# Optimization experiments

Hardware: AMD Instinct MI355X
Metric: run time of the kernel (lower is better)

## Reference

```python
import jax, jax.numpy as jnp
import numpy as np

# FP8 E4M3 constants (per FP8Handler)
E4M3_MAX = 240.0          # max_normal
MANTISSA_SCALE = 8.0      # 2 ** mantissa_bits (3)
SCALE_EPS = 1e-10


def setup_inputs() -> dict:
    key = jax.random.key(0)
    k1, k2, k3 = jax.random.split(key, 3)
    B, S, D_IN, D_OUT = 4, 2048, 4096, 4096
    x = jax.random.normal(k1, (B, S, D_IN), dtype=jnp.float32)
    weight = jax.random.normal(k2, (D_OUT, D_IN), dtype=jnp.float32)
    bias = jax.random.normal(k3, (D_OUT,), dtype=jnp.float32)
    return {"x": x, "weight": weight, "bias": bias}


def _fp8_e4m3_quant_dequant(w, scale):
    # FP8Handler.quantize_tensor + _simulate_e4m3_precision
    s = jnp.clip(w / scale, -E4M3_MAX, E4M3_MAX)
    s = s.astype(jnp.float16).astype(jnp.float32)  # fp16 round-trip
    q = jnp.round(s * MANTISSA_SCALE) / MANTISSA_SCALE  # mantissa truncation
    q = jnp.clip(q, -E4M3_MAX, E4M3_MAX)
    return q * scale


def reference(x, weight, bias):
    # FP8Quantizer.compute_scale: per-tensor max-abs, margin=0, fresh history
    amax = jnp.max(jnp.abs(weight))
    scale = jnp.maximum(amax / E4M3_MAX, SCALE_EPS)
    qw = _fp8_e4m3_quant_dequant(weight, scale)  # [out, in]
    # F.linear(x, qw, bias): x [b, s, in] @ qw.T [in, out] + bias
    return jnp.einsum('bsi,oi->bso', x, qw) + bias
```

## Files before the change

kernel.cpp:

```cpp
#include <hip/hip_runtime.h>
#include <hip/hip_bf16.h>
#include <hip/hip_fp16.h>

#define E4M3_MAX 240.0f

typedef __attribute__((ext_vector_type(8))) __bf16 bf16x8;
typedef __attribute__((ext_vector_type(16))) float f32x16;
typedef unsigned short ushort_t;

__device__ __forceinline__ void gload_lds16(const void* g, void* l) {
  __builtin_amdgcn_global_load_lds(
      (const __attribute__((address_space(1))) void*)g,
      (__attribute__((address_space(3))) void*)l,
      16, 0, 0);
}

__global__ void amax_abs_kernel(const float* __restrict__ w, int n4,
                                unsigned* __restrict__ amax_bits) {
  float m = 0.0f;
  const float4* w4 = (const float4*)w;
  int stride = gridDim.x * blockDim.x;
  for (int i = blockIdx.x * blockDim.x + threadIdx.x; i < n4; i += stride) {
    float4 v = w4[i];
    m = fmaxf(m, fmaxf(fmaxf(fabsf(v.x), fabsf(v.y)),
                       fmaxf(fabsf(v.z), fabsf(v.w))));
  }
  for (int off = 32; off > 0; off >>= 1)
    m = fmaxf(m, __shfl_down(m, off, 64));
  __shared__ float smax[4];
  int l = threadIdx.x & 63, wv = threadIdx.x >> 6;
  if (l == 0) smax[wv] = m;
  __syncthreads();
  if (threadIdx.x == 0) {
    float bm = fmaxf(fmaxf(smax[0], smax[1]), fmaxf(smax[2], smax[3]));
    atomicMax(amax_bits, __float_as_uint(bm));
  }
}

__global__ void quant_weight_kernel(const float* __restrict__ w,
                                    const unsigned* __restrict__ amax_bits,
                                    ushort_t* __restrict__ qw, int n4) {
  float amax = __uint_as_float(*amax_bits);
  float scale = fmaxf(amax / E4M3_MAX, 1e-10f);
  const float4* w4 = (const float4*)w;
  ushort4* q4 = (ushort4*)qw;
  int stride = gridDim.x * blockDim.x;
  for (int i = blockIdx.x * blockDim.x + threadIdx.x; i < n4; i += stride) {
    float4 v = w4[i];
    float r[4] = {v.x, v.y, v.z, v.w};
    ushort_t o[4];
#pragma unroll
    for (int j = 0; j < 4; ++j) {
      float s = fminf(fmaxf(r[j] / scale, -E4M3_MAX), E4M3_MAX);
      s = __half2float(__float2half(s));
      float q = rintf(s * 8.0f) * 0.125f;
      q = fminf(fmaxf(q, -E4M3_MAX), E4M3_MAX);
      __hip_bfloat16 h = __float2bfloat16(q * scale);
      o[j] = *(ushort_t*)&h;
    }
    ushort4 ov = {o[0], o[1], o[2], o[3]};
    q4[i] = ov;
  }
}

__global__ void cvt_bf16_kernel(const float* __restrict__ x,
                                ushort_t* __restrict__ xb, int n4) {
  const float4* x4 = (const float4*)x;
  ushort4* o4 = (ushort4*)xb;
  int stride = gridDim.x * blockDim.x;
  for (int i = blockIdx.x * blockDim.x + threadIdx.x; i < n4; i += stride) {
    float4 v = x4[i];
    __hip_bfloat16 h0 = __float2bfloat16(v.x);
    __hip_bfloat16 h1 = __float2bfloat16(v.y);
    __hip_bfloat16 h2 = __float2bfloat16(v.z);
    __hip_bfloat16 h3 = __float2bfloat16(v.w);
    ushort4 o = {*(ushort_t*)&h0, *(ushort_t*)&h1,
                 *(ushort_t*)&h2, *(ushort_t*)&h3};
    o4[i] = o;
  }
}


#define BAR() do { asm volatile("" ::: "memory"); \
                   __builtin_amdgcn_s_barrier(); \
                   asm volatile("" ::: "memory"); } while (0)
#define LGKM0() asm volatile("s_waitcnt lgkmcnt(0)" ::: "memory")
#define LGKM8() asm volatile("s_waitcnt lgkmcnt(8)" ::: "memory")
#define VMC8() asm volatile("s_waitcnt vmcnt(8)" ::: "memory")
#define VMC0() asm volatile("s_waitcnt vmcnt(0)" ::: "memory")
#define NOVM() do {} while (0)

__global__ __launch_bounds__(512, 2) void gemm256_p3(
    const ushort_t* __restrict__ A, const ushort_t* __restrict__ Bt,
    const float* __restrict__ bias, float* __restrict__ C) {
  constexpr int K = 4096, N = 4096;
  __shared__ __align__(16) ushort_t As[2][2][8192];
  __shared__ __align__(16) ushort_t Bs[2][2][8192];

  const int tid = threadIdx.x;
  const int wid = tid >> 6, lane = tid & 63;
  const int wm = wid >> 2, wn = wid & 3;
  const int l31 = lane & 31, lk2 = lane >> 5;

  int bid = blockIdx.x;
  int swz = (bid & 7) * 64 + (bid >> 3);
  int bm = swz >> 4, bn = swz & 15;

  const ushort_t* Ab = A + (size_t)bm * 256 * K;
  const ushort_t* Bb = Bt + (size_t)bn * 256 * K;

  int offG[2];
#pragma unroll
  for (int q = 0; q < 2; ++q) {
    int s = q * 512 + tid;
    int row = s >> 3;
    int c = (s & 7) ^ (row & 7) ^ ((row >> 3) & 3);
    offG[q] = row * K + c * 8;
  }

#define STAGE_AH(buf, kt, h)                                               \
  do { _Pragma("unroll") for (int q = 0; q < 2; ++q)                       \
    gload_lds16(Ab + (size_t)(h) * 128 * K + (kt) * 64 + offG[q],          \
                &As[buf][h][(q * 512 + wid * 64) * 8]); } while (0)
#define STAGE_BH(buf, kt, h)                                               \
  do { _Pragma("unroll") for (int q = 0; q < 2; ++q)                       \
    gload_lds16(Bb + (size_t)(h) * 128 * K + (kt) * 64 + offG[q],          \
                &Bs[buf][h][(q * 512 + wid * 64) * 8]); } while (0)

  const int bhalf = wn >> 1;
  const int brow0 = (wn & 1) * 64;
  const int sig = (l31 & 7) ^ ((l31 >> 3) & 3);
  int xks[4];
#pragma unroll
  for (int ks = 0; ks < 4; ++ks) xks[ks] = ((ks * 2 + lk2) ^ sig) * 8;

  bf16x8 af[4][4], bf[2][4];
  f32x16 acc[4][2] = {};

#define RD_A32(buf, rg)                                                    \
  do { _Pragma("unroll") for (int ks = 0; ks < 4; ++ks)                    \
    af[rg][ks] = *(const bf16x8*)                                          \
        &As[buf][wm][((rg) * 32 + l31) * 64 + xks[ks]]; } while (0)
#define RD_B32(buf)                                                        \
  do { _Pragma("unroll") for (int cg = 0; cg < 2; ++cg)                    \
    _Pragma("unroll") for (int ks = 0; ks < 4; ++ks)                       \
      bf[cg][ks] = *(const bf16x8*)                                        \
          &Bs[buf][bhalf][(brow0 + cg * 32 + l31) * 64 + xks[ks]]; } while (0)

#define MMA8(rg)                                                           \
  do { __builtin_amdgcn_s_setprio(1);                                      \
    _Pragma("unroll") for (int ks = 0; ks < 4; ++ks) {                     \
      acc[rg][0] = __builtin_amdgcn_mfma_f32_32x32x16_bf16(                \
          af[rg][ks], bf[0][ks], acc[rg][0], 0, 0, 0);                     \
      acc[rg][1] = __builtin_amdgcn_mfma_f32_32x32x16_bf16(                \
          af[rg][ks], bf[1][ks], acc[rg][1], 0, 0, 0);                     \
    }                                                                      \
    __builtin_amdgcn_s_setprio(0); } while (0)

#define TILE(cb, u, DO_S, VMCX)                                            \
  do {                                                                     \
    RD_B32(cb); RD_A32(cb, 0);                                             \
    LGKM8(); BAR(); LGKM0(); MMA8(0); BAR();                               \
    RD_A32(cb, 1); RD_A32(cb, 2); RD_A32(cb, 3);                           \
    if (DO_S) { STAGE_BH(cb, (u) + 2, 0); STAGE_BH(cb, (u) + 2, 1); }      \
    LGKM8(); BAR(); LGKM0(); MMA8(1); BAR();                               \
    if (DO_S) { STAGE_AH(cb, (u) + 2, 0); STAGE_AH(cb, (u) + 2, 1); }      \
    MMA8(2); MMA8(3);                                                      \
    VMCX; BAR();                                                           \
  } while (0)

  STAGE_BH(0, 0, 0); STAGE_BH(0, 0, 1);
  STAGE_AH(0, 0, 0); STAGE_AH(0, 0, 1);
  STAGE_BH(1, 1, 0); STAGE_BH(1, 1, 1);
  STAGE_AH(1, 1, 0); STAGE_AH(1, 1, 1);
  VMC8();
  BAR();

  for (int t = 0; t < 62; t += 2) {
    TILE(0, t, 1, VMC8());
    TILE(1, t + 1, 1, VMC8());
  }
  TILE(0, 62, 0, VMC0());
  TILE(1, 63, 0, NOVM());

  float* Cb = C + (size_t)(bm * 256 + wm * 128) * N + bn * 256 + wn * 64;
#pragma unroll
  for (int cg = 0; cg < 2; ++cg) {
    int n = cg * 32 + l31;
    float bv = bias[bn * 256 + wn * 64 + n];
#pragma unroll
    for (int rg = 0; rg < 4; ++rg) {
#pragma unroll
      for (int r = 0; r < 16; ++r) {
        int row = rg * 32 + (r & 3) + 8 * (r >> 2) + 4 * lk2;
        Cb[(size_t)row * N + n] = acc[rg][cg][r] + bv;
      }
    }
  }
}

extern "C" void kernel_launch(void* const* d_in, const int* in_sizes, int n_in,
                              void* d_out, int out_size, void* d_ws, size_t ws_size,
                              hipStream_t stream) {
  const float* x = (const float*)d_in[0];
  const float* wt = (const float*)d_in[1];
  const float* bias = (const float*)d_in[2];
  float* out = (float*)d_out;

  const int DIN = 4096;
  const int NW = in_sizes[1];
  const int M = in_sizes[0] / DIN;

  char* ws = (char*)d_ws;
  unsigned* amax_bits = (unsigned*)ws;
  ushort_t* qw = (ushort_t*)(ws + 256);
  ushort_t* xb = (ushort_t*)(ws + 256 + (size_t)NW * 2);

  hipMemsetAsync(amax_bits, 0, 4, stream);
  hipLaunchKernelGGL(amax_abs_kernel, dim3(1024), dim3(256), 0, stream,
                     wt, NW / 4, amax_bits);
  hipLaunchKernelGGL(quant_weight_kernel, dim3(2048), dim3(256), 0, stream,
                     wt, amax_bits, qw, NW / 4);
  hipLaunchKernelGGL(cvt_bf16_kernel, dim3(2048), dim3(256), 0, stream,
                     x, xb, (M * DIN) / 4);

  hipLaunchKernelGGL(gemm256_p3, dim3(512), dim3(512), 0, stream,
                     xb, qw, bias, out);
}
```

Measured before the change: 331.8 us.

## Restructure GEMM mainloop into 4-stage BK=32 pipeline with register double buffering

Replaces the 2-buffer BK=64 LDS pipeline with a 4-buffer BK=32 ring, so global-to-LDS loads are issued three tiles ahead. LDS fragments for the next tile are read into a second register set while MFMAs run on the current one, with a single barrier per tile and a sched_barrier to keep reads and MMAs apart. The intent is to hide LDS and global latency better and cut the multiple barriers per tile. In exchange it doubles the number of tile iterations and barriers across K, raises fragment register pressure, and changes the LDS swizzle to a 4-chunk pattern that may bank-conflict more.

```diff
diff --git a/kernel.cpp b/kernel.cpp
--- a/kernel.cpp
+++ b/kernel.cpp
@@ -84,18 +84,17 @@
 #define BAR() do { asm volatile("" ::: "memory"); \
                    __builtin_amdgcn_s_barrier(); \
                    asm volatile("" ::: "memory"); } while (0)
-#define LGKM0() asm volatile("s_waitcnt lgkmcnt(0)" ::: "memory")
-#define LGKM8() asm volatile("s_waitcnt lgkmcnt(8)" ::: "memory")
 #define VMC8() asm volatile("s_waitcnt vmcnt(8)" ::: "memory")
+#define VMC4() asm volatile("s_waitcnt vmcnt(4)" ::: "memory")
 #define VMC0() asm volatile("s_waitcnt vmcnt(0)" ::: "memory")
-#define NOVM() do {} while (0)
-
-__global__ __launch_bounds__(512, 2) void gemm256_p3(
+#define SB0()  __builtin_amdgcn_sched_barrier(0)
+
+__global__ __launch_bounds__(512, 2) void gemm256_pipe4(
     const ushort_t* __restrict__ A, const ushort_t* __restrict__ Bt,
     const float* __restrict__ bias, float* __restrict__ C) {
   constexpr int K = 4096, N = 4096;
-  __shared__ __align__(16) ushort_t As[2][2][8192];
-  __shared__ __align__(16) ushort_t Bs[2][2][8192];
+  __shared__ __align__(16) ushort_t As[4][2][4096];
+  __shared__ __align__(16) ushort_t Bs[4][2][4096];
 
   const int tid = threadIdx.x;
   const int wid = tid >> 6, lane = tid & 63;
@@ -113,75 +112,78 @@
 #pragma unroll
   for (int q = 0; q < 2; ++q) {
     int s = q * 512 + tid;
-    int row = s >> 3;
-    int c = (s & 7) ^ (row & 7) ^ ((row >> 3) & 3);
+    int row = s >> 2;
+    int c = (s & 3) ^ (row & 3) ^ ((row >> 2) & 3);
     offG[q] = row * K + c * 8;
   }
 
-#define STAGE_AH(buf, kt, h)                                               \
+#define STAGE_A(bufL, kt)                                                  \
   do { _Pragma("unroll") for (int q = 0; q < 2; ++q)                       \
-    gload_lds16(Ab + (size_t)(h) * 128 * K + (kt) * 64 + offG[q],          \
-                &As[buf][h][(q * 512 + wid * 64) * 8]); } while (0)
-#define STAGE_BH(buf, kt, h)                                               \
+    gload_lds16(Ab + (size_t)(kt) * 32 + offG[q],                          \
+                &As[bufL][q][tid * 8]); } while (0)
+#define STAGE_B(bufL, kt)                                                  \
   do { _Pragma("unroll") for (int q = 0; q < 2; ++q)                       \
-    gload_lds16(Bb + (size_t)(h) * 128 * K + (kt) * 64 + offG[q],          \
-                &Bs[buf][h][(q * 512 + wid * 64) * 8]); } while (0)
+    gload_lds16(Bb + (size_t)(kt) * 32 + offG[q],                          \
+                &Bs[bufL][q][tid * 8]); } while (0)
 
   const int bhalf = wn >> 1;
   const int brow0 = (wn & 1) * 64;
-  const int sig = (l31 & 7) ^ ((l31 >> 3) & 3);
-  int xks[4];
-#pragma unroll
-  for (int ks = 0; ks < 4; ++ks) xks[ks] = ((ks * 2 + lk2) ^ sig) * 8;
-
-  bf16x8 af[4][4], bf[2][4];
+  const int sig2 = (l31 & 3) ^ ((l31 >> 2) & 3);
+  int xk2[2];
+#pragma unroll
+  for (int ks = 0; ks < 2; ++ks) xk2[ks] = ((ks * 2 + lk2) ^ sig2) * 8;
+
+  bf16x8 af0[4][2], af1[4][2], bf0[2][2], bf1[2][2];
   f32x16 acc[4][2] = {};
 
-#define RD_A32(buf, rg)                                                    \
-  do { _Pragma("unroll") for (int ks = 0; ks < 4; ++ks)                    \
-    af[rg][ks] = *(const bf16x8*)                                          \
-        &As[buf][wm][((rg) * 32 + l31) * 64 + xks[ks]]; } while (0)
-#define RD_B32(buf)                                                        \
-  do { _Pragma("unroll") for (int cg = 0; cg < 2; ++cg)                    \
-    _Pragma("unroll") for (int ks = 0; ks < 4; ++ks)                       \
-      bf[cg][ks] = *(const bf16x8*)                                        \
-          &Bs[buf][bhalf][(brow0 + cg * 32 + l31) * 64 + xks[ks]]; } while (0)
-
-#define MMA8(rg)                                                           \
+#define RD12(S, bufL)                                                      \
+  do {                                                                     \
+    _Pragma("unroll") for (int cg = 0; cg < 2; ++cg)                       \
+      _Pragma("unroll") for (int ks = 0; ks < 2; ++ks)                     \
+        bf##S[cg][ks] = *(const bf16x8*)                                   \
+            &Bs[bufL][bhalf][(brow0 + cg * 32 + l31) * 32 + xk2[ks]];      \
+    _Pragma("unroll") for (int rg = 0; rg < 4; ++rg)                       \
+      _Pragma("unroll") for (int ks = 0; ks < 2; ++ks)                     \
+        af##S[rg][ks] = *(const bf16x8*)                                   \
+            &As[bufL][wm][((rg) * 32 + l31) * 32 + xk2[ks]];               \
+  } while (0)
+
+#define MMA16(S)                                                           \
   do { __builtin_amdgcn_s_setprio(1);                                      \
-    _Pragma("unroll") for (int ks = 0; ks < 4; ++ks) {                     \
-      acc[rg][0] = __builtin_amdgcn_mfma_f32_32x32x16_bf16(                \
-          af[rg][ks], bf[0][ks], acc[rg][0], 0, 0, 0);                     \
-      acc[rg][1] = __builtin_amdgcn_mfma_f32_32x32x16_bf16(                \
-          af[rg][ks], bf[1][ks], acc[rg][1], 0, 0, 0);                     \
-    }                                                                      \
+    _Pragma("unroll") for (int rg = 0; rg < 4; ++rg)                       \
+      _Pragma("unroll") for (int ks = 0; ks < 2; ++ks) {                   \
+        acc[rg][0] = __builtin_amdgcn_mfma_f32_32x32x16_bf16(              \
+            af##S[rg][ks], bf##S[0][ks], acc[rg][0], 0, 0, 0);             \
+        acc[rg][1] = __builtin_amdgcn_mfma_f32_32x32x16_bf16(              \
+            af##S[rg][ks], bf##S[1][ks], acc[rg][1], 0, 0, 0);             \
+      }                                                                    \
     __builtin_amdgcn_s_setprio(0); } while (0)
 
-#define TILE(cb, u, DO_S, VMCX)                                            \
+#define TILE(VMCX, DO_S, SBUF, skt, DO_R, RBUF, RS, CS)                    \
   do {                                                                     \
-    RD_B32(cb); RD_A32(cb, 0);                                             \
-    LGKM8(); BAR(); LGKM0(); MMA8(0); BAR();                               \
-    RD_A32(cb, 1); RD_A32(cb, 2); RD_A32(cb, 3);                           \
-    if (DO_S) { STAGE_BH(cb, (u) + 2, 0); STAGE_BH(cb, (u) + 2, 1); }      \
-    LGKM8(); BAR(); LGKM0(); MMA8(1); BAR();                               \
-    if (DO_S) { STAGE_AH(cb, (u) + 2, 0); STAGE_AH(cb, (u) + 2, 1); }      \
-    MMA8(2); MMA8(3);                                                      \
     VMCX; BAR();                                                           \
+    if (DO_S) { STAGE_A(SBUF, skt); STAGE_B(SBUF, skt); }                  \
+    if (DO_R) RD12(RS, RBUF);                                              \
+    SB0();                                                                 \
+    MMA16(CS);                                                             \
   } while (0)
 
-  STAGE_BH(0, 0, 0); STAGE_BH(0, 0, 1);
-  STAGE_AH(0, 0, 0); STAGE_AH(0, 0, 1);
-  STAGE_BH(1, 1, 0); STAGE_BH(1, 1, 1);
-  STAGE_AH(1, 1, 0); STAGE_AH(1, 1, 1);
-  VMC8();
-  BAR();
-
-  for (int t = 0; t < 62; t += 2) {
-    TILE(0, t, 1, VMC8());
-    TILE(1, t + 1, 1, VMC8());
-  }
-  TILE(0, 62, 0, VMC0());
-  TILE(1, 63, 0, NOVM());
+  STAGE_A(0, 0); STAGE_B(0, 0);
+  STAGE_A(1, 1); STAGE_B(1, 1);
+  STAGE_A(2, 2); STAGE_B(2, 2);
+  VMC8(); BAR();
+  RD12(0, 0);
+
+  for (int t = 0; t < 124; t += 4) {
+    TILE(VMC4(), 1, 3, t + 3, 1, 1, 1, 0);
+    TILE(VMC4(), 1, 0, t + 4, 1, 2, 0, 1);
+    TILE(VMC4(), 1, 1, t + 5, 1, 3, 1, 0);
+    TILE(VMC4(), 1, 2, t + 6, 1, 0, 0, 1);
+  }
+  TILE(VMC4(), 1, 3, 127, 1, 1, 1, 0);
+  TILE(VMC4(), 0, 0, 0,   1, 2, 0, 1);
+  TILE(VMC0(), 0, 0, 0,   1, 3, 1, 0);
+  MMA16(1);
 
   float* Cb = C + (size_t)(bm * 256 + wm * 128) * N + bn * 256 + wn * 64;
 #pragma unroll
@@ -224,6 +226,6 @@
   hipLaunchKernelGGL(cvt_bf16_kernel, dim3(2048), dim3(256), 0, stream,
                      x, xb, (M * DIN) / 4);
 
-  hipLaunchKernelGGL(gemm256_p3, dim3(512), dim3(512), 0, stream,
+  hipLaunchKernelGGL(gemm256_pipe4, dim3(512), dim3(512), 0, stream,
                      xb, qw, bias, out);
 }
```

New measurement: 362.4 us. 1.09x slower.

## Replace 256x256 GEMM tile with 128x128 tile and simpler double buffer

Applied to the files above, without the earlier changes.

Shrinks the GEMM block tile from 256x256 with 8 waves to 128x128 with 4 waves, launching 2048 blocks instead of 512. The k-loop becomes a plain double buffer that prefetches the next tile before reading the current one and waits with vmcnt(0) each step, replacing the interleaved half-tile staging. The aim is more blocks for better load balance and occupancy with less LDS per block. The cost is lower arithmetic intensity, so more global and L2 traffic per FLOP, and a full memory wait plus barrier every k-step.

```diff
diff --git a/kernel.cpp b/kernel.cpp
--- a/kernel.cpp
+++ b/kernel.cpp
@@ -84,68 +84,66 @@
 #define BAR() do { asm volatile("" ::: "memory"); \
                    __builtin_amdgcn_s_barrier(); \
                    asm volatile("" ::: "memory"); } while (0)
+#define FEN() asm volatile("" ::: "memory")
 #define LGKM0() asm volatile("s_waitcnt lgkmcnt(0)" ::: "memory")
-#define LGKM8() asm volatile("s_waitcnt lgkmcnt(8)" ::: "memory")
-#define VMC8() asm volatile("s_waitcnt vmcnt(8)" ::: "memory")
+#define LGKM4() asm volatile("s_waitcnt lgkmcnt(4)" ::: "memory")
 #define VMC0() asm volatile("s_waitcnt vmcnt(0)" ::: "memory")
 #define NOVM() do {} while (0)
 
-__global__ __launch_bounds__(512, 2) void gemm256_p3(
+__global__ __launch_bounds__(256, 2) void gemm128_2b(
     const ushort_t* __restrict__ A, const ushort_t* __restrict__ Bt,
     const float* __restrict__ bias, float* __restrict__ C) {
   constexpr int K = 4096, N = 4096;
-  __shared__ __align__(16) ushort_t As[2][2][8192];
-  __shared__ __align__(16) ushort_t Bs[2][2][8192];
+  __shared__ __align__(16) ushort_t As[2][8192];
+  __shared__ __align__(16) ushort_t Bs[2][8192];
 
   const int tid = threadIdx.x;
   const int wid = tid >> 6, lane = tid & 63;
-  const int wm = wid >> 2, wn = wid & 3;
+  const int wm = wid >> 1, wn = wid & 1;
   const int l31 = lane & 31, lk2 = lane >> 5;
 
   int bid = blockIdx.x;
-  int swz = (bid & 7) * 64 + (bid >> 3);
-  int bm = swz >> 4, bn = swz & 15;
-
-  const ushort_t* Ab = A + (size_t)bm * 256 * K;
-  const ushort_t* Bb = Bt + (size_t)bn * 256 * K;
-
-  int offG[2];
-#pragma unroll
-  for (int q = 0; q < 2; ++q) {
-    int s = q * 512 + tid;
+  int swz = (bid & 7) * 256 + (bid >> 3);
+  int bm = swz >> 5, bn = swz & 31;
+
+  const ushort_t* Ab = A + (size_t)bm * 128 * K;
+  const ushort_t* Bb = Bt + (size_t)bn * 128 * K;
+
+  int offG[4];
+#pragma unroll
+  for (int q = 0; q < 4; ++q) {
+    int s = q * 256 + tid;
     int row = s >> 3;
     int c = (s & 7) ^ (row & 7) ^ ((row >> 3) & 3);
     offG[q] = row * K + c * 8;
   }
 
-#define STAGE_AH(buf, kt, h)                                               \
-  do { _Pragma("unroll") for (int q = 0; q < 2; ++q)                       \
-    gload_lds16(Ab + (size_t)(h) * 128 * K + (kt) * 64 + offG[q],          \
-                &As[buf][h][(q * 512 + wid * 64) * 8]); } while (0)
-#define STAGE_BH(buf, kt, h)                                               \
-  do { _Pragma("unroll") for (int q = 0; q < 2; ++q)                       \
-    gload_lds16(Bb + (size_t)(h) * 128 * K + (kt) * 64 + offG[q],          \
-                &Bs[buf][h][(q * 512 + wid * 64) * 8]); } while (0)
-
-  const int bhalf = wn >> 1;
-  const int brow0 = (wn & 1) * 64;
+#define STAGE_A(buf, kt)                                                   \
+  do { _Pragma("unroll") for (int q = 0; q < 4; ++q)                       \
+    gload_lds16(Ab + (size_t)(kt) * 64 + offG[q],                          \
+                &As[buf][(q * 256 + tid) * 8 - lane * 8]); } while (0)
+#define STAGE_B(buf, kt)                                                   \
+  do { _Pragma("unroll") for (int q = 0; q < 4; ++q)                       \
+    gload_lds16(Bb + (size_t)(kt) * 64 + offG[q],                          \
+                &Bs[buf][(q * 256 + tid) * 8 - lane * 8]); } while (0)
+
   const int sig = (l31 & 7) ^ ((l31 >> 3) & 3);
   int xks[4];
 #pragma unroll
   for (int ks = 0; ks < 4; ++ks) xks[ks] = ((ks * 2 + lk2) ^ sig) * 8;
 
-  bf16x8 af[4][4], bf[2][4];
-  f32x16 acc[4][2] = {};
-
-#define RD_A32(buf, rg)                                                    \
-  do { _Pragma("unroll") for (int ks = 0; ks < 4; ++ks)                    \
-    af[rg][ks] = *(const bf16x8*)                                          \
-        &As[buf][wm][((rg) * 32 + l31) * 64 + xks[ks]]; } while (0)
-#define RD_B32(buf)                                                        \
+  bf16x8 af[2][4], bf[2][4];
+  f32x16 acc[2][2] = {};
+
+#define RD_B2(cb)                                                          \
   do { _Pragma("unroll") for (int cg = 0; cg < 2; ++cg)                    \
     _Pragma("unroll") for (int ks = 0; ks < 4; ++ks)                       \
       bf[cg][ks] = *(const bf16x8*)                                        \
-          &Bs[buf][bhalf][(brow0 + cg * 32 + l31) * 64 + xks[ks]]; } while (0)
+          &Bs[cb][(wn * 64 + cg * 32 + l31) * 64 + xks[ks]]; } while (0)
+#define RD_A1(cb, rg)                                                      \
+  do { _Pragma("unroll") for (int ks = 0; ks < 4; ++ks)                    \
+    af[rg][ks] = *(const bf16x8*)                                          \
+        &As[cb][(wm * 64 + (rg) * 32 + l31) * 64 + xks[ks]]; } while (0)
 
 #define MMA8(rg)                                                           \
   do { __builtin_amdgcn_s_setprio(1);                                      \
@@ -159,37 +157,32 @@
 
 #define TILE(cb, u, DO_S, VMCX)                                            \
   do {                                                                     \
-    RD_B32(cb); RD_A32(cb, 0);                                             \
-    LGKM8(); BAR(); LGKM0(); MMA8(0); BAR();                               \
-    RD_A32(cb, 1); RD_A32(cb, 2); RD_A32(cb, 3);                           \
-    if (DO_S) { STAGE_BH(cb, (u) + 2, 0); STAGE_BH(cb, (u) + 2, 1); }      \
-    LGKM8(); BAR(); LGKM0(); MMA8(1); BAR();                               \
-    if (DO_S) { STAGE_AH(cb, (u) + 2, 0); STAGE_AH(cb, (u) + 2, 1); }      \
-    MMA8(2); MMA8(3);                                                      \
+    if (DO_S) { STAGE_A((cb) ^ 1, (u) + 1); STAGE_B((cb) ^ 1, (u) + 1); }  \
+    RD_B2(cb); RD_A1(cb, 0); FEN();                                        \
+    RD_A1(cb, 1); FEN();                                                   \
+    LGKM4(); MMA8(0);                                                      \
+    LGKM0(); MMA8(1);                                                      \
     VMCX; BAR();                                                           \
   } while (0)
 
-  STAGE_BH(0, 0, 0); STAGE_BH(0, 0, 1);
-  STAGE_AH(0, 0, 0); STAGE_AH(0, 0, 1);
-  STAGE_BH(1, 1, 0); STAGE_BH(1, 1, 1);
-  STAGE_AH(1, 1, 0); STAGE_AH(1, 1, 1);
-  VMC8();
+  STAGE_A(0, 0); STAGE_B(0, 0);
+  VMC0();
   BAR();
 
-  for (int t = 0; t < 62; t += 2) {
-    TILE(0, t, 1, VMC8());
-    TILE(1, t + 1, 1, VMC8());
-  }
-  TILE(0, 62, 0, VMC0());
+  for (int u = 0; u < 62; u += 2) {
+    TILE(0, u, 1, VMC0());
+    TILE(1, u + 1, 1, VMC0());
+  }
+  TILE(0, 62, 1, VMC0());
   TILE(1, 63, 0, NOVM());
 
-  float* Cb = C + (size_t)(bm * 256 + wm * 128) * N + bn * 256 + wn * 64;
+  float* Cb = C + (size_t)(bm * 128 + wm * 64) * N + bn * 128 + wn * 64;
 #pragma unroll
   for (int cg = 0; cg < 2; ++cg) {
     int n = cg * 32 + l31;
-    float bv = bias[bn * 256 + wn * 64 + n];
-#pragma unroll
-    for (int rg = 0; rg < 4; ++rg) {
+    float bv = bias[bn * 128 + wn * 64 + n];
+#pragma unroll
+    for (int rg = 0; rg < 2; ++rg) {
 #pragma unroll
       for (int r = 0; r < 16; ++r) {
         int row = rg * 32 + (r & 3) + 8 * (r >> 2) + 4 * lk2;
@@ -224,6 +217,6 @@
   hipLaunchKernelGGL(cvt_bf16_kernel, dim3(2048), dim3(256), 0, stream,
                      x, xb, (M * DIN) / 4);
 
-  hipLaunchKernelGGL(gemm256_p3, dim3(512), dim3(512), 0, stream,
+  hipLaunchKernelGGL(gemm128_2b, dim3(2048), dim3(256), 0, stream,
                      xb, qw, bias, out);
 }
```

New measurement: 387.8 us. 16.9% more time.
